# Performance work log

Hardware: AMD Instinct MI355X
Metric: run time of the kernel (lower is better)

Reference implementation:

```python
import jax, jax.numpy as jnp
import numpy as np

B, T, D, H = 2, 2048, 1024, 16
HD = D // H


def sinusoidal_rel_pe(seq_len, d_model, dtype=jnp.float32):
    # Relative positions T-1 .. 0 (reversed), standard sin/cos interleave.
    pos = jnp.arange(seq_len - 1, -1, -1, dtype=jnp.float32)[:, None]  # [T,1]
    div = jnp.exp(-jnp.log(jnp.float32(10000.0)) * jnp.arange(0, d_model, 2, dtype=jnp.float32) / d_model)
    pe = jnp.zeros((seq_len, d_model), dtype=jnp.float32)
    pe = pe.at[:, 0::2].set(jnp.sin(pos * div))
    pe = pe.at[:, 1::2].set(jnp.cos(pos * div))
    return pe.astype(dtype)


def relative_to_absolute(x):
    # x: [B,H,T,L] with L == T. Music-Transformer skew trick.
    b, h, t1, l = x.shape
    x = jnp.pad(x, ((0, 0), (0, 0), (0, 0), (1, 0)))          # pad left of last dim
    x = x.reshape(b, h, -1)
    x = jnp.pad(x, ((0, 0), (0, 0), (l - t1, 0)))
    x = x.reshape(b, h, 1 + t1, l)
    return x[:, :, 1:]


def setup_inputs() -> dict:
    key = jax.random.key(0)
    k1, k2, k3 = jax.random.split(key, 3)
    x = jax.random.normal(k1, (B, T, D), dtype=jnp.float32)
    # causal mask: True where attention is disallowed (j > i)
    mask = jnp.triu(jnp.ones((T, T), dtype=bool), k=1)[None, None]
    mask = jnp.broadcast_to(mask, (B, 1, T, T))
    Wqkv = jax.random.normal(k2, (D, 3 * D), dtype=jnp.float32) * 0.02
    Wout = jax.random.normal(k3, (D, D), dtype=jnp.float32) * 0.02
    bout = jnp.zeros((D,), dtype=jnp.float32)
    return {"x": x, "mask": mask, "Wqkv": Wqkv, "Wout": Wout, "bout": bout}


def reference(x, mask, Wqkv, Wout, bout):
    b, t, d = x.shape
    scale = jnp.sqrt(jnp.float32(HD)).astype(x.dtype)
    qkv = x @ Wqkv                                  # [B,T,3D]
    q, k, v = jnp.split(qkv, 3, axis=-1)
    E = sinusoidal_rel_pe(t, d, x.dtype)            # [T,D], constant rel bias
    q = q.reshape(b, t, H, HD).transpose(0, 2, 1, 3)   # [B,H,T,hd]
    k = k.reshape(b, t, H, HD).transpose(0, 2, 1, 3)
    v = v.reshape(b, t, H, HD).transpose(0, 2, 1, 3)
    Eh = E.reshape(t, H, HD).transpose(1, 0, 2)        # [H,T,hd]
    att_k = jnp.einsum('bhqd,bhkd->bhqk', q, k)
    att_e = relative_to_absolute(jnp.einsum('bhqd,hkd->bhqk', q, Eh))
    score = (att_k + att_e) / scale
    score = jnp.where(mask, -jnp.inf, score)
    score = jax.nn.softmax(score, axis=-1)          # dropout is identity (eval)
    ctx = jnp.einsum('bhqk,bhkd->bhqd', score, v)
    ctx = ctx.transpose(0, 2, 1, 3).reshape(b, t, d)
    out = ctx @ Wout + bout
    return (out, score)
```

## Files before the change

kernel.cpp:

```cpp
#include <hip/hip_runtime.h>

typedef __bf16 bf16x8 __attribute__((ext_vector_type(8)));
typedef float f32x4 __attribute__((ext_vector_type(4)));

#define B_ 2
#define T_ 2048
#define D_ 1024
#define H_ 16

__device__ __forceinline__ ushort f2bf(float f) {
  union { float f; unsigned u; } v; v.f = f;
  unsigned u = v.u;
  return (ushort)((u + 0x7FFFu + ((u >> 16) & 1u)) >> 16);
}

__device__ __forceinline__ void g2l16(const void* g, void* l) {
  __builtin_amdgcn_global_load_lds(
      (const __attribute__((address_space(1))) unsigned int*)g,
      (__attribute__((address_space(3))) unsigned int*)l, 16, 0, 0);
}

__global__ __launch_bounds__(256) void cvt_kernel(const float* __restrict__ in,
                                                  ushort* __restrict__ out) {
  int i = (blockIdx.x * 256 + threadIdx.x) * 4;
  float4 v = *(const float4*)(in + i);
  ushort4 o;
  o.x = f2bf(v.x); o.y = f2bf(v.y); o.z = f2bf(v.z); o.w = f2bf(v.w);
  *(ushort4*)(out + i) = o;
}

__global__ void transpose_cvt(const float* __restrict__ in, ushort* __restrict__ out,
                              int R, int C) {
  __shared__ float tile[32][33];
  int bx = blockIdx.x * 32, by = blockIdx.y * 32;
  int tx = threadIdx.x, ty = threadIdx.y;
  for (int i = 0; i < 32; i += 8)
    tile[ty + i][tx] = in[(size_t)(by + ty + i) * C + (bx + tx)];
  __syncthreads();
  for (int i = 0; i < 32; i += 8)
    out[(size_t)(bx + ty + i) * R + (by + tx)] = f2bf(tile[tx][ty + i]);
}

__global__ __launch_bounds__(256) void gemm_bf16(
    const ushort* __restrict__ A, const ushort* __restrict__ BT,
    float* __restrict__ C, const float* __restrict__ bias,
    int M, int N, int K) {
  __shared__ alignas(16) ushort As[2][4096];
  __shared__ alignas(16) ushort Bs[2][4096];
  int tid = threadIdx.x;
  int wave = tid >> 6, lane = tid & 63;
  int l16 = lane & 15, lhi = lane >> 4;
  int m0 = blockIdx.y * 128, n0 = blockIdx.x * 128;
  int wr = (wave >> 1) * 64, wc = (wave & 1) * 64;
  int srow = lane >> 2, sch = lane & 3;

  f32x4 acc[4][4] = {};

  auto stage = [&](int kk, int buf) {
    for (int i = 0; i < 2; ++i) {
      int rg = i * 4 + wave;
      const ushort* ga = A + (size_t)(m0 + rg * 16 + srow) * K + kk + sch * 8;
      const ushort* gb = BT + (size_t)(n0 + rg * 16 + srow) * K + kk + sch * 8;
      g2l16(ga, &As[buf][rg * 512]);
      g2l16(gb, &Bs[buf][rg * 512]);
    }
  };

  stage(0, 0);
  int buf = 0;
  for (int kk = 0; kk < K; kk += 32) {
    __syncthreads();
    if (kk + 32 < K) stage(kk + 32, buf ^ 1);
    const ushort* Asb = As[buf];
    const ushort* Bsb = Bs[buf];
    bf16x8 af[4], bfr[4];
    for (int f = 0; f < 4; ++f)
      af[f] = *(const bf16x8*)(Asb + (wr + f * 16 + l16) * 32 + lhi * 8);
    for (int f = 0; f < 4; ++f)
      bfr[f] = *(const bf16x8*)(Bsb + (wc + f * 16 + l16) * 32 + lhi * 8);
    for (int fm = 0; fm < 4; ++fm)
      for (int fn = 0; fn < 4; ++fn)
        acc[fm][fn] = __builtin_amdgcn_mfma_f32_16x16x32_bf16(af[fm], bfr[fn], acc[fm][fn], 0, 0, 0);
    buf ^= 1;
  }
  for (int fm = 0; fm < 4; ++fm)
    for (int fn = 0; fn < 4; ++fn)
      for (int r = 0; r < 4; ++r) {
        int row = m0 + wr + fm * 16 + lhi * 4 + r;
        int col = n0 + wc + fn * 16 + l16;
        float v = acc[fm][fn][r];
        if (bias) v += bias[col];
        C[(size_t)row * N + col] = v;
      }
}

__global__ __launch_bounds__(256) void augment_kernel(
    const float* __restrict__ qkv,
    ushort* __restrict__ Qaug, ushort* __restrict__ Kaug, ushort* __restrict__ Vb) {
  int row = blockIdx.x;
  int b = row >> 11;
  int t = row & 2047;
  int tid = threadIdx.x;
  const float* src = qkv + (size_t)row * 3072;
  for (int i = 0; i < 4; ++i) {
    int idx = tid + i * 256;
    int h = idx >> 6, d = idx & 63;
    size_t obase = ((size_t)(b * H_ + h) * T_ + t);
    float q = src[idx];
    float k = src[1024 + idx];
    float v = src[2048 + idx];
    Qaug[obase * 128 + d] = f2bf(q * 0.125f);
    Kaug[obase * 128 + d] = f2bf(k);
    Vb[obase * 64 + d] = f2bf(v);
  }
  for (int i = 0; i < 2; ++i) {
    int idx = tid + i * 256;
    int h = idx >> 5, mm = idx & 31;
    int gdim = h * 64 + 2 * mm;
    float w = __expf(-9.2103403719761836f * (float)gdim * (1.0f / 1024.0f));
    float ang = w * (float)t;
    float si, co;
    __sincosf(ang, &si, &co);
    float qs = src[h * 64 + 2 * mm], qc = src[h * 64 + 2 * mm + 1];
    size_t obase = ((size_t)(b * H_ + h) * T_ + t);
    Qaug[obase * 128 + 64 + 2 * mm]     = f2bf((qs * si + qc * co) * 0.125f);
    Qaug[obase * 128 + 64 + 2 * mm + 1] = f2bf((qc * si - qs * co) * 0.125f);
    Kaug[obase * 128 + 64 + 2 * mm]     = f2bf(co);
    Kaug[obase * 128 + 64 + 2 * mm + 1] = f2bf(si);
  }
}

__global__ __launch_bounds__(256) void transpose_v(const ushort* __restrict__ Vb,
                                                   ushort* __restrict__ Vt) {
  __shared__ ushort tile[64][72];
  int bh = blockIdx.y, t0 = blockIdx.x * 64;
  int tid = threadIdx.x;
  for (int i = 0; i < 2; ++i) {
    int e = tid + i * 256;
    int row = e >> 3, ch = e & 7;
    *(int4*)(&tile[row][ch * 8]) =
        *(const int4*)(Vb + ((size_t)bh * T_ + t0 + row) * 64 + ch * 8);
  }
  __syncthreads();
  for (int i = 0; i < 2; ++i) {
    int e = tid + i * 256;
    int d = e >> 3, ch = e & 7;
    union { int4 v; ushort u[8]; } pk;
    for (int u = 0; u < 8; ++u) pk.u[u] = tile[ch * 8 + u][d];
    *(int4*)(Vt + ((size_t)bh * 64 + d) * T_ + t0 + ch * 8) = pk.v;
  }
}

__global__ __launch_bounds__(256) void attn_kernel(
    const ushort* __restrict__ Qaug,
    const ushort* __restrict__ Kaug,
    const ushort* __restrict__ Vt,
    float* __restrict__ score,
    ushort* __restrict__ ctxb) {
  int qt = 31 - blockIdx.x;
  int bh = blockIdx.y;
  int tid = threadIdx.x;
  int wave = tid >> 6, lane = tid & 63;
  int l16 = lane & 15, lhi = lane >> 4;
  int qb = wave * 16;
  int e7 = l16 & 7;

  __shared__ alignas(16) ushort Ks[2][8192];
  __shared__ alignas(16) ushort Vs[2][4096];
  __shared__ alignas(16) ushort Ps[2][4096];

  const ushort* Kbase = Kaug + (size_t)bh * T_ * 128;
  const ushort* Vbase = Vt + (size_t)bh * 64 * T_;

  auto stageK = [&](int kt, int buf) {
    for (int i = 0; i < 4; ++i) {
      int rg = i * 4 + wave;
      int key = rg * 4 + (lane >> 4);
      const ushort* g = Kbase + ((size_t)(kt * 64 + key)) * 128 + (((lane & 15) ^ (key & 7)) << 3);
      g2l16(g, &Ks[buf][rg * 512]);
    }
  };
  auto stageV = [&](int kt, int buf) {
    for (int i = 0; i < 2; ++i) {
      int rg = i * 4 + wave;
      int dim = rg * 8 + (lane >> 3);
      const ushort* g = Vbase + (size_t)dim * T_ + kt * 64 + (((lane & 7) ^ (dim & 7)) << 3);
      g2l16(g, &Vs[buf][rg * 512]);
    }
  };

  bf16x8 qf[4];
  {
    const ushort* Qg = Qaug + ((size_t)bh * T_ + qt * 64 + qb + l16) * 128;
    for (int ks = 0; ks < 4; ++ks)
      qf[ks] = *(const bf16x8*)(Qg + ks * 32 + lhi * 8);
  }

  stageK(0, 0);
  float plsum[4] = {0.f, 0.f, 0.f, 0.f};
  for (int kt = 0; kt <= qt; ++kt) {
    int buf = kt & 1;
    __syncthreads();
    if (kt < qt) stageK(kt + 1, buf ^ 1);
    const ushort* Kb = Ks[buf];
    f32x4 s[4] = {};
    for (int ks = 0; ks < 4; ++ks)
      for (int fn = 0; fn < 4; ++fn) {
        bf16x8 bfr = *(const bf16x8*)(Kb + (fn * 16 + l16) * 128 + ((((ks << 2) | lhi) ^ e7) << 3));
        s[fn] = __builtin_amdgcn_mfma_f32_16x16x32_bf16(qf[ks], bfr, s[fn], 0, 0, 0);
      }
    if (kt == qt) {
      for (int fn = 0; fn < 4; ++fn)
        for (int r = 0; r < 4; ++r)
          if (fn * 16 + l16 > qb + lhi * 4 + r) s[fn][r] = -1e30f;
    }
    for (int r = 0; r < 4; ++r)
      plsum[r] += __expf(s[0][r]) + __expf(s[1][r]) + __expf(s[2][r]) + __expf(s[3][r]);
  }
  float invl[4];
  for (int r = 0; r < 4; ++r) {
    float v = plsum[r];
    for (int dd = 1; dd < 16; dd <<= 1) v += __shfl_xor(v, dd);
    invl[r] = 1.f / v;
  }

  __syncthreads();
  stageK(0, 0);
  stageV(0, 0);
  f32x4 cacc[4] = {};
  float* srow = score + ((size_t)bh * T_ + (size_t)qt * 64) * T_;

  for (int kt = 0; kt <= qt; ++kt) {
    int buf = kt & 1;
    __syncthreads();
    if (kt < qt) { stageK(kt + 1, buf ^ 1); stageV(kt + 1, buf ^ 1); }
    const ushort* Kb = Ks[buf];
    f32x4 s[4] = {};
    for (int ks = 0; ks < 4; ++ks)
      for (int fn = 0; fn < 4; ++fn) {
        bf16x8 bfr = *(const bf16x8*)(Kb + (fn * 16 + l16) * 128 + ((((ks << 2) | lhi) ^ e7) << 3));
        s[fn] = __builtin_amdgcn_mfma_f32_16x16x32_bf16(qf[ks], bfr, s[fn], 0, 0, 0);
      }
    if (kt == qt) {
      for (int fn = 0; fn < 4; ++fn)
        for (int r = 0; r < 4; ++r)
          if (fn * 16 + l16 > qb + lhi * 4 + r) s[fn][r] = -1e30f;
    }
    ushort* Pb = Ps[buf];
    for (int fn = 0; fn < 4; ++fn)
      for (int r = 0; r < 4; ++r) {
        int row_loc = qb + lhi * 4 + r;
        float p = __expf(s[fn][r]) * invl[r];
        srow[(size_t)row_loc * T_ + kt * 64 + fn * 16 + l16] = p;
        Pb[row_loc * 64 + (((fn * 2 + (l16 >> 3)) ^ (row_loc & 7)) << 3) + e7] = f2bf(p);
      }
    asm volatile("s_waitcnt lgkmcnt(0)" ::: "memory");
    __builtin_amdgcn_sched_barrier(0);
    const ushort* Vb2 = Vs[buf];
    for (int ks = 0; ks < 2; ++ks) {
      bf16x8 pa = *(const bf16x8*)(Pb + (qb + l16) * 64 + ((((ks << 2) | lhi) ^ e7) << 3));
      for (int fn = 0; fn < 4; ++fn) {
        bf16x8 vb = *(const bf16x8*)(Vb2 + (fn * 16 + l16) * 64 + ((((ks << 2) | lhi) ^ e7) << 3));
        cacc[fn] = __builtin_amdgcn_mfma_f32_16x16x32_bf16(pa, vb, cacc[fn], 0, 0, 0);
      }
    }
  }

  {
    int row = tid >> 2, c16 = (tid & 3) * 16;
    float4 z = {0.f, 0.f, 0.f, 0.f};
    for (int kt = qt + 1; kt < 32; ++kt) {
      float* dst = srow + (size_t)row * T_ + kt * 64 + c16;
      for (int u = 0; u < 4; ++u) ((float4*)dst)[u] = z;
    }
  }

  int b = bh >> 4, h = bh & 15;
  for (int fn = 0; fn < 4; ++fn)
    for (int r = 0; r < 4; ++r) {
      int t = qt * 64 + qb + lhi * 4 + r;
      int col = h * 64 + fn * 16 + l16;
      ctxb[((size_t)(b * T_ + t)) * 1024 + col] = f2bf(cacc[fn][r]);
    }
}

extern "C" void kernel_launch(void* const* d_in, const int* in_sizes, int n_in,
                              void* d_out, int out_size, void* d_ws, size_t ws_size,
                              hipStream_t stream) {
  const float* x    = (const float*)d_in[0];
  const float* Wqkv = (const float*)d_in[2];
  const float* Wout = (const float*)d_in[3];
  const float* bout = (const float*)d_in[4];

  char* ws = (char*)d_ws;
  ushort* xb    = (ushort*)(ws + 0);
  ushort* wqkvT = (ushort*)(ws + 8388608);
  ushort* woutT = (ushort*)(ws + 14680064);
  float*  qkv   = (float*) (ws + 16777216);
  ushort* Qaug  = (ushort*)(ws + 67108864);
  ushort* Kaug  = (ushort*)(ws + 83886080);
  ushort* Vb    = (ushort*)(ws + 100663296);
  ushort* ctxb  = (ushort*)(ws + 109051904);
  ushort* Vt    = (ushort*)(ws + 16777216);

  float* out   = (float*)d_out;
  float* score = out + (size_t)4194304;

  cvt_kernel<<<4096, 256, 0, stream>>>(x, xb);
  dim3 tb(32, 8);
  transpose_cvt<<<dim3(3072 / 32, 1024 / 32), tb, 0, stream>>>(Wqkv, wqkvT, 1024, 3072);
  transpose_cvt<<<dim3(1024 / 32, 1024 / 32), tb, 0, stream>>>(Wout, woutT, 1024, 1024);
  gemm_bf16<<<dim3(24, 32), 256, 0, stream>>>(xb, wqkvT, qkv, nullptr, 4096, 3072, 1024);
  augment_kernel<<<4096, 256, 0, stream>>>(qkv, Qaug, Kaug, Vb);
  transpose_v<<<dim3(32, 32), 256, 0, stream>>>(Vb, Vt);
  attn_kernel<<<dim3(32, 32), 256, 0, stream>>>(Qaug, Kaug, Vt, score, ctxb);
  gemm_bf16<<<dim3(8, 32), 256, 0, stream>>>(ctxb, woutT, out, bout, 4096, 1024, 1024);
}
```

Measured before the change: 329.8 us.

## Fuse QKV augmentation and V transpose into the QKV GEMM epilogue

The QKV projection GEMM now writes its outputs directly as bf16 Qaug (including the rotated sin/cos relative-position half), Kaug and transposed V. This removes the fp32 qkv intermediate, the augment kernel and the V transpose kernel. The K trig columns are filled by a small separate kernel, and the attention grid is remapped so that consecutive workgroups interleave across heads. The cost is a heavier GEMM epilogue with per-element sincos, lane shuffles and scattered 2-byte stores.

```diff
diff --git a/kernel.cpp b/kernel.cpp
--- a/kernel.cpp
+++ b/kernel.cpp
@@ -7,6 +7,7 @@
 #define T_ 2048
 #define D_ 1024
 #define H_ 16
+#define NLOG4 -9.2103403719761836f
 
 __device__ __forceinline__ ushort f2bf(float f) {
   union { float f; unsigned u; } v; v.f = f;
@@ -41,10 +42,22 @@
     out[(size_t)(bx + ty + i) * R + (by + tx)] = f2bf(tile[tx][ty + i]);
 }
 
-__global__ __launch_bounds__(256) void gemm_bf16(
+__global__ __launch_bounds__(512) void fill_ktrig(ushort* __restrict__ Kaug) {
+  int t = blockIdx.x;
+  int tid = threadIdx.x;
+  int h = tid >> 5, mm = tid & 31;
+  float w = __expf(NLOG4 * (float)(h * 64 + 2 * mm) * (1.0f / 1024.0f));
+  float si, co;
+  __sincosf(w * (float)t, &si, &co);
+  ushort2 pk;
+  pk.x = f2bf(co); pk.y = f2bf(si);
+  for (int b = 0; b < 2; ++b)
+    *(ushort2*)(Kaug + (((size_t)(b * H_ + h) * T_ + t) * 128 + 64 + 2 * mm)) = pk;
+}
+
+__global__ __launch_bounds__(256) void gemm_qkv(
     const ushort* __restrict__ A, const ushort* __restrict__ BT,
-    float* __restrict__ C, const float* __restrict__ bias,
-    int M, int N, int K) {
+    ushort* __restrict__ Qaug, ushort* __restrict__ Kaug, ushort* __restrict__ Vt) {
   __shared__ alignas(16) ushort As[2][4096];
   __shared__ alignas(16) ushort Bs[2][4096];
   int tid = threadIdx.x;
@@ -53,16 +66,15 @@
   int m0 = blockIdx.y * 128, n0 = blockIdx.x * 128;
   int wr = (wave >> 1) * 64, wc = (wave & 1) * 64;
   int srow = lane >> 2, sch = lane & 3;
+  const int K = 1024;
 
   f32x4 acc[4][4] = {};
 
   auto stage = [&](int kk, int buf) {
     for (int i = 0; i < 2; ++i) {
       int rg = i * 4 + wave;
-      const ushort* ga = A + (size_t)(m0 + rg * 16 + srow) * K + kk + sch * 8;
-      const ushort* gb = BT + (size_t)(n0 + rg * 16 + srow) * K + kk + sch * 8;
-      g2l16(ga, &As[buf][rg * 512]);
-      g2l16(gb, &Bs[buf][rg * 512]);
+      g2l16(A + (size_t)(m0 + rg * 16 + srow) * K + kk + sch * 8, &As[buf][rg * 512]);
+      g2l16(BT + (size_t)(n0 + rg * 16 + srow) * K + kk + sch * 8, &Bs[buf][rg * 512]);
     }
   };
 
@@ -83,6 +95,81 @@
         acc[fm][fn] = __builtin_amdgcn_mfma_f32_16x16x32_bf16(af[fm], bfr[fn], acc[fm][fn], 0, 0, 0);
     buf ^= 1;
   }
+
+  int slice = n0 >> 10;
+  bool odd = l16 & 1;
+  for (int fn = 0; fn < 4; ++fn) {
+    int col = n0 + wc + fn * 16 + l16;
+    int d = col & 1023;
+    int h = d >> 6, hd = d & 63;
+    float w = (slice == 0) ? __expf(NLOG4 * (float)(d & ~1) * (1.0f / 1024.0f)) : 0.f;
+    for (int fm = 0; fm < 4; ++fm) {
+      int row0 = m0 + wr + fm * 16 + lhi * 4;
+      int b = row0 >> 11, t0 = row0 & 2047;
+      size_t obase = ((size_t)(b * H_ + h) * T_ + t0);
+      if (slice == 0) {
+        for (int r = 0; r < 4; ++r) {
+          float qv = acc[fm][fn][r];
+          float prt = __shfl_xor(qv, 1);
+          float si, co;
+          __sincosf(w * (float)(t0 + r), &si, &co);
+          float val = odd ? (qv * si - prt * co) : (qv * si + prt * co);
+          Qaug[(obase + r) * 128 + hd] = f2bf(qv * 0.125f);
+          Qaug[(obase + r) * 128 + 64 + hd] = f2bf(val * 0.125f);
+        }
+      } else if (slice == 1) {
+        for (int r = 0; r < 4; ++r)
+          Kaug[(obase + r) * 128 + hd] = f2bf(acc[fm][fn][r]);
+      } else {
+        ushort4 pk;
+        pk.x = f2bf(acc[fm][fn][0]); pk.y = f2bf(acc[fm][fn][1]);
+        pk.z = f2bf(acc[fm][fn][2]); pk.w = f2bf(acc[fm][fn][3]);
+        *(ushort4*)(Vt + ((size_t)(b * H_ + h) * 64 + hd) * T_ + t0) = pk;
+      }
+    }
+  }
+}
+
+__global__ __launch_bounds__(256) void gemm_bf16(
+    const ushort* __restrict__ A, const ushort* __restrict__ BT,
+    float* __restrict__ C, const float* __restrict__ bias,
+    int M, int N, int K) {
+  __shared__ alignas(16) ushort As[2][4096];
+  __shared__ alignas(16) ushort Bs[2][4096];
+  int tid = threadIdx.x;
+  int wave = tid >> 6, lane = tid & 63;
+  int l16 = lane & 15, lhi = lane >> 4;
+  int m0 = blockIdx.y * 128, n0 = blockIdx.x * 128;
+  int wr = (wave >> 1) * 64, wc = (wave & 1) * 64;
+  int srow = lane >> 2, sch = lane & 3;
+
+  f32x4 acc[4][4] = {};
+
+  auto stage = [&](int kk, int buf) {
+    for (int i = 0; i < 2; ++i) {
+      int rg = i * 4 + wave;
+      g2l16(A + (size_t)(m0 + rg * 16 + srow) * K + kk + sch * 8, &As[buf][rg * 512]);
+      g2l16(BT + (size_t)(n0 + rg * 16 + srow) * K + kk + sch * 8, &Bs[buf][rg * 512]);
+    }
+  };
+
+  stage(0, 0);
+  int buf = 0;
+  for (int kk = 0; kk < K; kk += 32) {
+    __syncthreads();
+    if (kk + 32 < K) stage(kk + 32, buf ^ 1);
+    const ushort* Asb = As[buf];
+    const ushort* Bsb = Bs[buf];
+    bf16x8 af[4], bfr[4];
+    for (int f = 0; f < 4; ++f)
+      af[f] = *(const bf16x8*)(Asb + (wr + f * 16 + l16) * 32 + lhi * 8);
+    for (int f = 0; f < 4; ++f)
+      bfr[f] = *(const bf16x8*)(Bsb + (wc + f * 16 + l16) * 32 + lhi * 8);
+    for (int fm = 0; fm < 4; ++fm)
+      for (int fn = 0; fn < 4; ++fn)
+        acc[fm][fn] = __builtin_amdgcn_mfma_f32_16x16x32_bf16(af[fm], bfr[fn], acc[fm][fn], 0, 0, 0);
+    buf ^= 1;
+  }
   for (int fm = 0; fm < 4; ++fm)
     for (int fn = 0; fn < 4; ++fn)
       for (int r = 0; r < 4; ++r) {
@@ -94,71 +181,16 @@
       }
 }
 
-__global__ __launch_bounds__(256) void augment_kernel(
-    const float* __restrict__ qkv,
-    ushort* __restrict__ Qaug, ushort* __restrict__ Kaug, ushort* __restrict__ Vb) {
-  int row = blockIdx.x;
-  int b = row >> 11;
-  int t = row & 2047;
-  int tid = threadIdx.x;
-  const float* src = qkv + (size_t)row * 3072;
-  for (int i = 0; i < 4; ++i) {
-    int idx = tid + i * 256;
-    int h = idx >> 6, d = idx & 63;
-    size_t obase = ((size_t)(b * H_ + h) * T_ + t);
-    float q = src[idx];
-    float k = src[1024 + idx];
-    float v = src[2048 + idx];
-    Qaug[obase * 128 + d] = f2bf(q * 0.125f);
-    Kaug[obase * 128 + d] = f2bf(k);
-    Vb[obase * 64 + d] = f2bf(v);
-  }
-  for (int i = 0; i < 2; ++i) {
-    int idx = tid + i * 256;
-    int h = idx >> 5, mm = idx & 31;
-    int gdim = h * 64 + 2 * mm;
-    float w = __expf(-9.2103403719761836f * (float)gdim * (1.0f / 1024.0f));
-    float ang = w * (float)t;
-    float si, co;
-    __sincosf(ang, &si, &co);
-    float qs = src[h * 64 + 2 * mm], qc = src[h * 64 + 2 * mm + 1];
-    size_t obase = ((size_t)(b * H_ + h) * T_ + t);
-    Qaug[obase * 128 + 64 + 2 * mm]     = f2bf((qs * si + qc * co) * 0.125f);
-    Qaug[obase * 128 + 64 + 2 * mm + 1] = f2bf((qc * si - qs * co) * 0.125f);
-    Kaug[obase * 128 + 64 + 2 * mm]     = f2bf(co);
-    Kaug[obase * 128 + 64 + 2 * mm + 1] = f2bf(si);
-  }
-}
-
-__global__ __launch_bounds__(256) void transpose_v(const ushort* __restrict__ Vb,
-                                                   ushort* __restrict__ Vt) {
-  __shared__ ushort tile[64][72];
-  int bh = blockIdx.y, t0 = blockIdx.x * 64;
-  int tid = threadIdx.x;
-  for (int i = 0; i < 2; ++i) {
-    int e = tid + i * 256;
-    int row = e >> 3, ch = e & 7;
-    *(int4*)(&tile[row][ch * 8]) =
-        *(const int4*)(Vb + ((size_t)bh * T_ + t0 + row) * 64 + ch * 8);
-  }
-  __syncthreads();
-  for (int i = 0; i < 2; ++i) {
-    int e = tid + i * 256;
-    int d = e >> 3, ch = e & 7;
-    union { int4 v; ushort u[8]; } pk;
-    for (int u = 0; u < 8; ++u) pk.u[u] = tile[ch * 8 + u][d];
-    *(int4*)(Vt + ((size_t)bh * 64 + d) * T_ + t0 + ch * 8) = pk.v;
-  }
-}
-
 __global__ __launch_bounds__(256) void attn_kernel(
     const ushort* __restrict__ Qaug,
     const ushort* __restrict__ Kaug,
     const ushort* __restrict__ Vt,
     float* __restrict__ score,
     ushort* __restrict__ ctxb) {
-  int qt = 31 - blockIdx.x;
-  int bh = blockIdx.y;
+  int flat = blockIdx.y * 32 + blockIdx.x;
+  int wg = (flat & 7) * 128 + (flat >> 3);
+  int bh = wg >> 5;
+  int qt = 31 - (wg & 31);
   int tid = threadIdx.x;
   int wave = tid >> 6, lane = tid & 63;
   int l16 = lane & 15, lhi = lane >> 4;
@@ -296,12 +328,10 @@
   ushort* xb    = (ushort*)(ws + 0);
   ushort* wqkvT = (ushort*)(ws + 8388608);
   ushort* woutT = (ushort*)(ws + 14680064);
-  float*  qkv   = (float*) (ws + 16777216);
-  ushort* Qaug  = (ushort*)(ws + 67108864);
-  ushort* Kaug  = (ushort*)(ws + 83886080);
-  ushort* Vb    = (ushort*)(ws + 100663296);
-  ushort* ctxb  = (ushort*)(ws + 109051904);
-  ushort* Vt    = (ushort*)(ws + 16777216);
+  ushort* Qaug  = (ushort*)(ws + 16777216);
+  ushort* Kaug  = (ushort*)(ws + 33554432);
+  ushort* Vt    = (ushort*)(ws + 50331648);
+  ushort* ctxb  = (ushort*)(ws + 58720256);
 
   float* out   = (float*)d_out;
   float* score = out + (size_t)4194304;
@@ -310,9 +340,8 @@
   dim3 tb(32, 8);
   transpose_cvt<<<dim3(3072 / 32, 1024 / 32), tb, 0, stream>>>(Wqkv, wqkvT, 1024, 3072);
   transpose_cvt<<<dim3(1024 / 32, 1024 / 32), tb, 0, stream>>>(Wout, woutT, 1024, 1024);
-  gemm_bf16<<<dim3(24, 32), 256, 0, stream>>>(xb, wqkvT, qkv, nullptr, 4096, 3072, 1024);
-  augment_kernel<<<4096, 256, 0, stream>>>(qkv, Qaug, Kaug, Vb);
-  transpose_v<<<dim3(32, 32), 256, 0, stream>>>(Vb, Vt);
+  fill_ktrig<<<2048, 512, 0, stream>>>(Kaug);
+  gemm_qkv<<<dim3(24, 32), 256, 0, stream>>>(xb, wqkvT, Qaug, Kaug, Vt);
   attn_kernel<<<dim3(32, 32), 256, 0, stream>>>(Qaug, Kaug, Vt, score, ctxb);
   gemm_bf16<<<dim3(8, 32), 256, 0, stream>>>(ctxb, woutT, out, bout, 4096, 1024, 1024);
 }
```

After: 686.9 us. +108.3%, slower.
